# Performance work log

Measured on AMD Instinct MI355X. Metric: run time of the kernel, lower is better.

## Reference

```python
import jax, jax.numpy as jnp
import numpy as np

B, N, D = 16, 4096, 128          # graphs, points per graph, feature dim
RATIO = 0.25
M = int(N * RATIO)               # 1024 sampled points per graph (static)
RADIUS = 0.2


def setup_inputs() -> dict:
    key = jax.random.key(0)
    k1, k2 = jax.random.split(key)
    x = jax.random.normal(k1, (B * N, D), dtype=jnp.float32)
    pos = jax.random.uniform(k2, (B * N, 3), dtype=jnp.float32)  # unit cube
    batch = jnp.repeat(jnp.arange(B, dtype=jnp.int32), N)        # sorted, equal-size graphs
    return {"x": x, "pos": pos, "batch": batch}


def _fps(pos_g):
    """Farthest point sampling on one graph. pos_g: [N,3] -> [M] int indices.
    Deterministic start at index 0 (random_start=False, i.e. eval mode)."""
    def step(carry, _):
        dist, last = carry
        d = jnp.sum((pos_g - pos_g[last]) ** 2, axis=-1)   # [N]
        dist = jnp.minimum(dist, d)                        # dist to nearest selected
        nxt = jnp.argmax(dist).astype(jnp.int32)
        return (dist, nxt), last
    init = (jnp.full((pos_g.shape[0],), jnp.inf, pos_g.dtype), jnp.int32(0))
    _, idx = jax.lax.scan(step, init, None, length=M)
    return idx  # [M]


def reference(x, pos, batch):
    # Equal-size graphs -> reshape instead of segment bookkeeping.
    pos_b = pos.reshape(B, N, 3)
    x_b = x.reshape(B, N, D)

    # FPS per graph, vmapped (sequential greedy selection inside lax.scan).
    idx = jax.vmap(_fps)(pos_b)                                    # [B, M]

    sampled_pos = jnp.take_along_axis(pos_b, idx[:, :, None], axis=1)  # [B, M, 3]
    sampled_x = jnp.take_along_axis(x_b, idx[:, :, None], axis=1)      # [B, M, D]

    # radius_graph within each graph: boolean adjacency (j within r of i, no self loops).
    diff = sampled_pos[:, :, None, :] - sampled_pos[:, None, :, :]     # [B, M, M, 3]
    d2 = jnp.sum(diff * diff, axis=-1)                                 # [B, M, M]
    adj = (d2 <= RADIUS * RADIUS) & ~jnp.eye(M, dtype=bool)[None]      # [B, M, M]

    sampled_batch = jnp.repeat(jnp.arange(B, dtype=batch.dtype), M)    # [B*M]
    return (sampled_x.reshape(B * M, D),
            sampled_pos.reshape(B * M, 3),
            sampled_batch,
            adj)
```

## Files before the change

### kernel.cpp

```cpp
#include <hip/hip_runtime.h>
#include <stdint.h>

#define BB 16
#define NN 4096
#define DD 128
#define MM 1024
#define RADIUS2 0.04f
#define TPB 256
#define PPT 16
#define NPAIR (PPT / 2)
#define NW  (TPB / 64)

typedef unsigned long long u64;
typedef unsigned int u32;
typedef float f32x2 __attribute__((ext_vector_type(2)));
typedef unsigned int uint2v __attribute__((ext_vector_type(2)));

__device__ __forceinline__ u32 umin2(u32 a, u32 b) { return a < b ? a : b; }
__device__ __forceinline__ u32 umin3(u32 a, u32 b, u32 c) { return umin2(umin2(a, b), c); }
__device__ __forceinline__ float fmax3(float a, float b, float c) { return fmaxf(fmaxf(a, b), c); }

template <int CTRL>
__device__ __forceinline__ float dpp_fmax(float v) {
    int o = __builtin_amdgcn_update_dpp(0, __float_as_int(v), CTRL, 0xF, 0xF, true);
    return fmaxf(v, __int_as_float(o));
}
__device__ __forceinline__ float wave_fmax(float v) {
    v = dpp_fmax<0xB1>(v);
    v = dpp_fmax<0x4E>(v);
    v = dpp_fmax<0x141>(v);
    v = dpp_fmax<0x140>(v);
    { int o = __builtin_amdgcn_ds_swizzle(__float_as_int(v), 0x401F); v = fmaxf(v, __int_as_float(o)); }
#if __has_builtin(__builtin_amdgcn_permlane32_swap)
    { uint2v r = __builtin_amdgcn_permlane32_swap(__float_as_uint(v), __float_as_uint(v), false, false);
      v = fmaxf(__uint_as_float(r[0]), __uint_as_float(r[1])); }
#else
    v = fmaxf(v, __shfl_xor(v, 32, 64));
#endif
    return v;
}
template <int CTRL>
__device__ __forceinline__ u32 dpp_umin(u32 v) {
    u32 o = (u32)__builtin_amdgcn_update_dpp(0, (int)v, CTRL, 0xF, 0xF, true);
    return umin2(v, o);
}
__device__ __forceinline__ u32 wave_umin(u32 v) {
    v = dpp_umin<0xB1>(v);
    v = dpp_umin<0x4E>(v);
    v = dpp_umin<0x141>(v);
    v = dpp_umin<0x140>(v);
    { u32 o = (u32)__builtin_amdgcn_ds_swizzle((int)v, 0x401F); v = umin2(v, o); }
#if __has_builtin(__builtin_amdgcn_permlane32_swap)
    { uint2v r = __builtin_amdgcn_permlane32_swap(v, v, false, false); v = umin2(r[0], r[1]); }
#else
    v = umin2(v, __shfl_xor(v, 32, 64));
#endif
    return v;
}

__global__ __launch_bounds__(TPB) void fps_kernel(const float* __restrict__ pos,
                                                  int* __restrict__ idx_out) {
    const int b    = blockIdx.x;
    const int tid  = threadIdx.x;
    const int wid  = tid >> 6;
    const int lane = tid & 63;

    __shared__ float4 pos4[NN];
    __shared__ u64 partials[2][NW];

    const float* pg = pos + (size_t)b * NN * 3;
    for (int k = tid; k < NN * 3; k += TPB)
        ((float*)&pos4[k / 3])[k % 3] = pg[k];
    __syncthreads();

    f32x2 px[NPAIR], py[NPAIR], pz[NPAIR];
    float dist[PPT];
    u32 idxs[PPT];
#pragma unroll
    for (int j = 0; j < NPAIR; ++j) {
        float4 a = pos4[tid * PPT + 2 * j];
        float4 c = pos4[tid * PPT + 2 * j + 1];
        px[j] = (f32x2){a.x, c.x};
        py[j] = (f32x2){a.y, c.y};
        pz[j] = (f32x2){a.z, c.z};
    }
#pragma unroll
    for (int k = 0; k < PPT; ++k) {
        dist[k] = __builtin_inff();
        idxs[k] = (u32)(tid * PPT + k);
    }

    int last = 0;

    for (int m = 0; m < MM; ++m) {
        if (tid == 0) idx_out[b * MM + m] = last;
        if (m == MM - 1) break;

        float4 lp = pos4[last];
        f32x2 lx = {lp.x, lp.x}, ly = {lp.y, lp.y}, lz = {lp.z, lp.z};

        {
#pragma clang fp contract(off)
#pragma unroll
            for (int j = 0; j < NPAIR; ++j) {
                f32x2 dx = px[j] - lx;
                f32x2 dy = py[j] - ly;
                f32x2 dz = pz[j] - lz;
                f32x2 d  = dx * dx + dy * dy;
                d = d + dz * dz;
                dist[2 * j]     = fminf(dist[2 * j],     d.x);
                dist[2 * j + 1] = fminf(dist[2 * j + 1], d.y);
            }
        }

        float t0 = fmax3(dist[0],  dist[1],  dist[2]);
        float t1 = fmax3(dist[3],  dist[4],  dist[5]);
        float t2 = fmax3(dist[6],  dist[7],  dist[8]);
        float t3 = fmax3(dist[9],  dist[10], dist[11]);
        float t4 = fmax3(dist[12], dist[13], dist[14]);
        float tmax = fmax3(fmax3(t0, t1, t2), fmaxf(t3, t4), dist[15]);

        float wmax = wave_fmax(tmax);

        u32 c[PPT];
#pragma unroll
        for (int k = 0; k < PPT; ++k)
            c[k] = (dist[k] == wmax) ? idxs[k] : 0xFFFFFFFFu;
        u32 s0 = umin3(c[0],  c[1],  c[2]);
        u32 s1 = umin3(c[3],  c[4],  c[5]);
        u32 s2 = umin3(c[6],  c[7],  c[8]);
        u32 s3 = umin3(c[9],  c[10], c[11]);
        u32 s4 = umin3(c[12], c[13], c[14]);
        u32 cand = umin3(umin3(s0, s1, s2), umin2(s3, s4), c[15]);

        u32 widx = wave_umin(cand);

        const int buf = m & 1;
        if (lane == 0)
            partials[buf][wid] = ((u64)__float_as_uint(wmax) << 32) | (u64)widx;
        __syncthreads();

        u64 e0 = partials[buf][0];
        u64 e1 = partials[buf][1];
        u64 e2 = partials[buf][2];
        u64 e3 = partials[buf][3];
        float m0 = __uint_as_float((u32)(e0 >> 32));
        float m1 = __uint_as_float((u32)(e1 >> 32));
        float m2 = __uint_as_float((u32)(e2 >> 32));
        float m3 = __uint_as_float((u32)(e3 >> 32));
        float g  = fmaxf(fmaxf(m0, m1), fmaxf(m2, m3));
        u32 li = (u32)e3;
        li = (m2 == g) ? (u32)e2 : li;
        li = (m1 == g) ? (u32)e1 : li;
        li = (m0 == g) ? (u32)e0 : li;
        last = (int)li;
    }
}

__global__ void gather_x_kernel(const float* __restrict__ x,
                                const int* __restrict__ idx,
                                float* __restrict__ out) {
    int t = blockIdx.x * blockDim.x + threadIdx.x;
    if (t >= BB * MM * DD / 4) return;
    int row = t >> 5;
    int c4  = (t & 31) << 2;
    int b   = row >> 10;
    int n   = idx[row];
    const float4 v = *(const float4*)(x + ((size_t)(b * NN + n) * DD + c4));
    *(float4*)(out + (size_t)row * DD + c4) = v;
}

__global__ void gather_pb_kernel(const float* __restrict__ pos,
                                 const int* __restrict__ idx,
                                 float* __restrict__ spos,
                                 float* __restrict__ sbatch) {
    int r = blockIdx.x * blockDim.x + threadIdx.x;
    if (r >= BB * MM) return;
    int b = r >> 10;
    int n = idx[r];
    const float* p = pos + (size_t)(b * NN + n) * 3;
    spos[r * 3 + 0] = p[0];
    spos[r * 3 + 1] = p[1];
    spos[r * 3 + 2] = p[2];
    sbatch[r] = (float)b;
}

__global__ void adj_kernel(const float* __restrict__ spos,
                           float* __restrict__ adj) {
    int row = blockIdx.x;
    int b   = row >> 10;
    int i   = row & (MM - 1);
    const float* pb = spos + (size_t)b * MM * 3;
    float xi = pb[i * 3 + 0];
    float yi = pb[i * 3 + 1];
    float zi = pb[i * 3 + 2];

    int j0 = threadIdx.x << 2;
    float4 r;
    float* o = adj + (size_t)row * MM;
#pragma unroll
    for (int k = 0; k < 4; ++k) {
        int j = j0 + k;
        float dx = xi - pb[j * 3 + 0];
        float dy = yi - pb[j * 3 + 1];
        float dz = zi - pb[j * 3 + 2];
        float d2 = __fadd_rn(__fadd_rn(__fmul_rn(dx, dx), __fmul_rn(dy, dy)),
                             __fmul_rn(dz, dz));
        float v = (d2 <= RADIUS2 && j != i) ? 1.0f : 0.0f;
        ((float*)&r)[k] = v;
    }
    *(float4*)(o + j0) = r;
}

extern "C" void kernel_launch(void* const* d_in, const int* in_sizes, int n_in,
                              void* d_out, int out_size, void* d_ws, size_t ws_size,
                              hipStream_t stream) {
    const float* x   = (const float*)d_in[0];
    const float* pos = (const float*)d_in[1];

    float* out    = (float*)d_out;
    int*   idx_ws = (int*)d_ws;

    float* sx   = out;
    float* spos = sx + (size_t)BB * MM * DD;
    float* sbat = spos + (size_t)BB * MM * 3;
    float* adj  = sbat + (size_t)BB * MM;

    fps_kernel<<<BB, TPB, 0, stream>>>(pos, idx_ws);
    gather_x_kernel<<<(BB * MM * DD / 4 + 255) / 256, 256, 0, stream>>>(x, idx_ws, sx);
    gather_pb_kernel<<<(BB * MM + 255) / 256, 256, 0, stream>>>(pos, idx_ws, spos, sbat);
    adj_kernel<<<BB * MM, 256, 0, stream>>>(spos, adj);
}
```

Before: 690.0 us.

## Restructure FPS argmax to publish winner coordinates and shorten the per-iteration critical path

Each thread now finds its local argmax slot and prefetches that point's coordinates from LDS before the wave reduction, so the wave argmin operates on one candidate per thread. The winning lane writes the max, its xyz and its index into shared memory, so after the barrier every thread takes the next point's coordinates directly and skips a dependent LDS load of pos4[last]. Distances are kept as packed float2 with a vector min, and the xor-16 step uses permlane16_swap when the builtin exists. This targets the serial latency of each of the 1023 dependent iterations, at the cost of an extra LDS read per thread per iteration and more shared-memory writes.

After: 718.7 us. +4.1%, slower.

```diff
diff --git a/kernel.cpp b/kernel.cpp
--- a/kernel.cpp
+++ b/kernel.cpp
@@ -25,57 +25,82 @@
     int o = __builtin_amdgcn_update_dpp(0, __float_as_int(v), CTRL, 0xF, 0xF, true);
     return fmaxf(v, __int_as_float(o));
 }
+template <int CTRL>
+__device__ __forceinline__ u32 dpp_umin(u32 v) {
+    u32 o = (u32)__builtin_amdgcn_update_dpp(0, (int)v, CTRL, 0xF, 0xF, true);
+    return umin2(v, o);
+}
+
+__device__ __forceinline__ float xor16_fmax(float v) {
+#if __has_builtin(__builtin_amdgcn_permlane16_swap)
+    uint2v r = __builtin_amdgcn_permlane16_swap(__float_as_uint(v), __float_as_uint(v), false, false);
+    return fmaxf(__uint_as_float(r[0]), __uint_as_float(r[1]));
+#else
+    int o = __builtin_amdgcn_ds_swizzle(__float_as_int(v), 0x401F);
+    return fmaxf(v, __int_as_float(o));
+#endif
+}
+__device__ __forceinline__ u32 xor16_umin(u32 v) {
+#if __has_builtin(__builtin_amdgcn_permlane16_swap)
+    uint2v r = __builtin_amdgcn_permlane16_swap(v, v, false, false);
+    return umin2(r[0], r[1]);
+#else
+    u32 o = (u32)__builtin_amdgcn_ds_swizzle((int)v, 0x401F);
+    return umin2(v, o);
+#endif
+}
+__device__ __forceinline__ float xor32_fmax(float v) {
+#if __has_builtin(__builtin_amdgcn_permlane32_swap)
+    uint2v r = __builtin_amdgcn_permlane32_swap(__float_as_uint(v), __float_as_uint(v), false, false);
+    return fmaxf(__uint_as_float(r[0]), __uint_as_float(r[1]));
+#else
+    return fmaxf(v, __shfl_xor(v, 32, 64));
+#endif
+}
+__device__ __forceinline__ u32 xor32_umin(u32 v) {
+#if __has_builtin(__builtin_amdgcn_permlane32_swap)
+    uint2v r = __builtin_amdgcn_permlane32_swap(v, v, false, false);
+    return umin2(r[0], r[1]);
+#else
+    return umin2(v, __shfl_xor(v, 32, 64));
+#endif
+}
+
 __device__ __forceinline__ float wave_fmax(float v) {
     v = dpp_fmax<0xB1>(v);
     v = dpp_fmax<0x4E>(v);
     v = dpp_fmax<0x141>(v);
     v = dpp_fmax<0x140>(v);
-    { int o = __builtin_amdgcn_ds_swizzle(__float_as_int(v), 0x401F); v = fmaxf(v, __int_as_float(o)); }
-#if __has_builtin(__builtin_amdgcn_permlane32_swap)
-    { uint2v r = __builtin_amdgcn_permlane32_swap(__float_as_uint(v), __float_as_uint(v), false, false);
-      v = fmaxf(__uint_as_float(r[0]), __uint_as_float(r[1])); }
-#else
-    v = fmaxf(v, __shfl_xor(v, 32, 64));
-#endif
+    v = xor16_fmax(v);
+    v = xor32_fmax(v);
     return v;
-}
-template <int CTRL>
-__device__ __forceinline__ u32 dpp_umin(u32 v) {
-    u32 o = (u32)__builtin_amdgcn_update_dpp(0, (int)v, CTRL, 0xF, 0xF, true);
-    return umin2(v, o);
 }
 __device__ __forceinline__ u32 wave_umin(u32 v) {
     v = dpp_umin<0xB1>(v);
     v = dpp_umin<0x4E>(v);
     v = dpp_umin<0x141>(v);
     v = dpp_umin<0x140>(v);
-    { u32 o = (u32)__builtin_amdgcn_ds_swizzle((int)v, 0x401F); v = umin2(v, o); }
-#if __has_builtin(__builtin_amdgcn_permlane32_swap)
-    { uint2v r = __builtin_amdgcn_permlane32_swap(v, v, false, false); v = umin2(r[0], r[1]); }
-#else
-    v = umin2(v, __shfl_xor(v, 32, 64));
-#endif
+    v = xor16_umin(v);
+    v = xor32_umin(v);
     return v;
 }
 
 __global__ __launch_bounds__(TPB) void fps_kernel(const float* __restrict__ pos,
                                                   int* __restrict__ idx_out) {
-    const int b    = blockIdx.x;
-    const int tid  = threadIdx.x;
-    const int wid  = tid >> 6;
-    const int lane = tid & 63;
+    const int b   = blockIdx.x;
+    const int tid = threadIdx.x;
+    const int wid = tid >> 6;
 
     __shared__ float4 pos4[NN];
-    __shared__ u64 partials[2][NW];
+    __shared__ float4 fpart[2][NW];
+    __shared__ u32    ipart[2][NW];
 
     const float* pg = pos + (size_t)b * NN * 3;
     for (int k = tid; k < NN * 3; k += TPB)
         ((float*)&pos4[k / 3])[k % 3] = pg[k];
     __syncthreads();
 
-    f32x2 px[NPAIR], py[NPAIR], pz[NPAIR];
-    float dist[PPT];
-    u32 idxs[PPT];
+    f32x2 px[NPAIR], py[NPAIR], pz[NPAIR], dist2[NPAIR];
 #pragma unroll
     for (int j = 0; j < NPAIR; ++j) {
         float4 a = pos4[tid * PPT + 2 * j];
@@ -83,77 +108,83 @@
         px[j] = (f32x2){a.x, c.x};
         py[j] = (f32x2){a.y, c.y};
         pz[j] = (f32x2){a.z, c.z};
+        dist2[j] = (f32x2){__builtin_inff(), __builtin_inff()};
     }
-#pragma unroll
-    for (int k = 0; k < PPT; ++k) {
-        dist[k] = __builtin_inff();
-        idxs[k] = (u32)(tid * PPT + k);
-    }
-
-    int last = 0;
-
-    for (int m = 0; m < MM; ++m) {
-        if (tid == 0) idx_out[b * MM + m] = last;
-        if (m == MM - 1) break;
-
-        float4 lp = pos4[last];
-        f32x2 lx = {lp.x, lp.x}, ly = {lp.y, lp.y}, lz = {lp.z, lp.z};
-
+
+    if (tid == 0) idx_out[b * MM] = 0;
+    float4 lp = pos4[0];
+    float lx = lp.x, ly = lp.y, lz = lp.z;
+
+    for (int m = 1; m < MM; ++m) {
         {
 #pragma clang fp contract(off)
+            f32x2 vx = {lx, lx}, vy = {ly, ly}, vz = {lz, lz};
 #pragma unroll
             for (int j = 0; j < NPAIR; ++j) {
-                f32x2 dx = px[j] - lx;
-                f32x2 dy = py[j] - ly;
-                f32x2 dz = pz[j] - lz;
+                f32x2 dx = px[j] - vx;
+                f32x2 dy = py[j] - vy;
+                f32x2 dz = pz[j] - vz;
                 f32x2 d  = dx * dx + dy * dy;
                 d = d + dz * dz;
-                dist[2 * j]     = fminf(dist[2 * j],     d.x);
-                dist[2 * j + 1] = fminf(dist[2 * j + 1], d.y);
+                dist2[j] = __builtin_elementwise_min(dist2[j], d);
             }
         }
 
-        float t0 = fmax3(dist[0],  dist[1],  dist[2]);
-        float t1 = fmax3(dist[3],  dist[4],  dist[5]);
-        float t2 = fmax3(dist[6],  dist[7],  dist[8]);
-        float t3 = fmax3(dist[9],  dist[10], dist[11]);
-        float t4 = fmax3(dist[12], dist[13], dist[14]);
-        float tmax = fmax3(fmax3(t0, t1, t2), fmaxf(t3, t4), dist[15]);
+        float t0 = fmaxf(dist2[0].x, dist2[0].y);
+        float t1 = fmaxf(dist2[1].x, dist2[1].y);
+        float t2 = fmaxf(dist2[2].x, dist2[2].y);
+        float t3 = fmaxf(dist2[3].x, dist2[3].y);
+        float t4 = fmaxf(dist2[4].x, dist2[4].y);
+        float t5 = fmaxf(dist2[5].x, dist2[5].y);
+        float t6 = fmaxf(dist2[6].x, dist2[6].y);
+        float t7 = fmaxf(dist2[7].x, dist2[7].y);
+        float tmax = fmax3(fmax3(t0, t1, t2), fmax3(t3, t4, t5), fmaxf(t6, t7));
+
+        u32 c[PPT];
+#pragma unroll
+        for (int j = 0; j < NPAIR; ++j) {
+            c[2 * j]     = (dist2[j].x == tmax) ? (u32)(2 * j)     : 64u;
+            c[2 * j + 1] = (dist2[j].y == tmax) ? (u32)(2 * j + 1) : 64u;
+        }
+        u32 a0 = umin3(c[0],  c[1],  c[2]);
+        u32 a1 = umin3(c[3],  c[4],  c[5]);
+        u32 a2 = umin3(c[6],  c[7],  c[8]);
+        u32 a3 = umin3(c[9],  c[10], c[11]);
+        u32 a4 = umin3(c[12], c[13], c[14]);
+        u32 sl = umin3(umin3(a0, a1, a2), umin2(a3, a4), c[15]);
+        u32 gidx = (u32)(tid * PPT) + sl;
+
+        float4 sp = pos4[gidx];
 
         float wmax = wave_fmax(tmax);
-
-        u32 c[PPT];
-#pragma unroll
-        for (int k = 0; k < PPT; ++k)
-            c[k] = (dist[k] == wmax) ? idxs[k] : 0xFFFFFFFFu;
-        u32 s0 = umin3(c[0],  c[1],  c[2]);
-        u32 s1 = umin3(c[3],  c[4],  c[5]);
-        u32 s2 = umin3(c[6],  c[7],  c[8]);
-        u32 s3 = umin3(c[9],  c[10], c[11]);
-        u32 s4 = umin3(c[12], c[13], c[14]);
-        u32 cand = umin3(umin3(s0, s1, s2), umin2(s3, s4), c[15]);
-
+        u32 cand = (tmax == wmax) ? gidx : 0xFFFFFFFFu;
         u32 widx = wave_umin(cand);
 
         const int buf = m & 1;
-        if (lane == 0)
-            partials[buf][wid] = ((u64)__float_as_uint(wmax) << 32) | (u64)widx;
+        if (cand == widx) {
+            fpart[buf][wid] = make_float4(wmax, sp.x, sp.y, sp.z);
+            ipart[buf][wid] = widx;
+        }
         __syncthreads();
 
-        u64 e0 = partials[buf][0];
-        u64 e1 = partials[buf][1];
-        u64 e2 = partials[buf][2];
-        u64 e3 = partials[buf][3];
-        float m0 = __uint_as_float((u32)(e0 >> 32));
-        float m1 = __uint_as_float((u32)(e1 >> 32));
-        float m2 = __uint_as_float((u32)(e2 >> 32));
-        float m3 = __uint_as_float((u32)(e3 >> 32));
-        float g  = fmaxf(fmaxf(m0, m1), fmaxf(m2, m3));
-        u32 li = (u32)e3;
-        li = (m2 == g) ? (u32)e2 : li;
-        li = (m1 == g) ? (u32)e1 : li;
-        li = (m0 == g) ? (u32)e0 : li;
-        last = (int)li;
+        float4 q0 = fpart[buf][0];
+        float4 q1 = fpart[buf][1];
+        float4 q2 = fpart[buf][2];
+        float4 q3 = fpart[buf][3];
+        float g = fmaxf(fmaxf(q0.x, q1.x), fmaxf(q2.x, q3.x));
+        float nx = q3.y, ny = q3.z, nz = q3.w;
+        bool b2 = (q2.x == g); nx = b2 ? q2.y : nx; ny = b2 ? q2.z : ny; nz = b2 ? q2.w : nz;
+        bool b1 = (q1.x == g); nx = b1 ? q1.y : nx; ny = b1 ? q1.z : ny; nz = b1 ? q1.w : nz;
+        bool b0 = (q0.x == g); nx = b0 ? q0.y : nx; ny = b0 ? q0.z : ny; nz = b0 ? q0.w : nz;
+        lx = nx; ly = ny; lz = nz;
+
+        if (tid == 0) {
+            u32 li = ipart[buf][3];
+            li = b2 ? ipart[buf][2] : li;
+            li = b1 ? ipart[buf][1] : li;
+            li = b0 ? ipart[buf][0] : li;
+            idx_out[b * MM + m] = (int)li;
+        }
     }
 }
 
```
